# Optimization experiments

Measured on AMD Instinct MI355X. Metric: run time of the kernel, lower is better.

## Reference

```python
import jax, jax.numpy as jnp
import numpy as np
from jax import lax

K, N = 256, 65536

def setup_inputs() -> dict:
    key = jax.random.key(0)
    k1, k2, k3 = jax.random.split(key, 3)
    # obs: non-negative event counts [K, N]
    obs = jax.random.uniform(k1, (K, N), dtype=jnp.float32) * 4.0
    # Beta ~ U(1, 3) [K]
    Beta = 1.0 + 2.0 * jax.random.uniform(k2, (K,), dtype=jnp.float32)
    # Alpha ~ U(0, 0.01) [K, K]
    Alpha = 0.01 * jax.random.uniform(k3, (K, K), dtype=jnp.float32)
    return {"obs": obs, "Beta": Beta, "Alpha": Alpha}

def reference(obs, Beta, Alpha):
    # obs: [K, N], Beta: [K], Alpha: [K, K]
    Kk, Nn = obs.shape
    Mu0 = obs.mean(axis=1) / 10.0 + 0.01            # [K] background rate
    decay = jnp.exp(-Beta)                          # [K]

    # Exponential kernel sum S[t] = sum_{tp<t} obs[:,tp] * Beta * exp(-(t-tp)*Beta)
    # admits recursion H[t] = exp(-Beta) * (H[t-1] + obs[:, t-1]), S[t] = Beta * H[t]
    def step(h, o_prev):
        h_new = decay * (h + o_prev)
        return h_new, h_new

    _, H = lax.scan(step, jnp.zeros((Kk,), obs.dtype), obs[:, :Nn - 1].T)  # [N-1, K]
    S = H * Beta                                    # [N-1, K]
    # lam1[:, t] = softplus(Alpha @ S[t]) for t >= 1; lam1[:, 0] = 0 (by original code)
    lam = jax.nn.softplus(jnp.einsum('jk,tk->tj', Alpha, S))  # [N-1, K]
    lams1 = jnp.concatenate([jnp.zeros((Kk, 1), obs.dtype), lam.T], axis=1)  # [K, N]
    lams0 = jnp.broadcast_to(Mu0[:, None], (Kk, Nn))          # [K, N]

    Nloglams = obs * jnp.log(lams0 + lams1 + 1e-5)
    loglik = (Nloglams - lams0 - lams1).sum()
    return loglik, lams0, lams1
```

## Files before the change

### kernel.cpp

```cpp
#include <hip/hip_runtime.h>
#include <math.h>

#define KK 256
#define NN 65536
#define TT 64
#define WW 48
#define TPAD 264

typedef __bf16 bf16x8 __attribute__((ext_vector_type(8)));
typedef float f32x4 __attribute__((ext_vector_type(4)));

__global__ __launch_bounds__(256) void rowsum_kernel(const float* __restrict__ obs,
                                                     float* __restrict__ partial) {
  const int b = blockIdx.x;
  const int r = b >> 3, e = b & 7;
  const int tid = threadIdx.x;
  const float4* p = (const float4*)(obs + (size_t)r * NN + e * 8192) + tid;
  float s = 0.f;
#pragma unroll
  for (int i = 0; i < 8; ++i) {
    float4 v = p[i * 256];
    s += (v.x + v.y) + (v.z + v.w);
  }
  __shared__ float red[256];
  red[tid] = s;
  __syncthreads();
  for (int off = 128; off > 0; off >>= 1) {
    if (tid < off) red[tid] += red[tid + off];
    __syncthreads();
  }
  if (tid == 0) partial[b] = red[0];
}

__global__ __launch_bounds__(256) void prep_kernel(const float* __restrict__ Alpha,
                                                   const float* __restrict__ partial,
                                                   float* __restrict__ mu0,
                                                   __bf16* __restrict__ AlphaB,
                                                   float* __restrict__ out) {
  const int j = blockIdx.x;
  const int tid = threadIdx.x;
  AlphaB[(size_t)j * KK + tid] = (__bf16)Alpha[(size_t)j * KK + tid];
  if (tid == 0) {
    float s = 0.f;
#pragma unroll
    for (int i = 0; i < 8; ++i) s += partial[j * 8 + i];
    mu0[j] = s * (1.0f / NN) * 0.1f + 0.01f;
    if (j == 0) out[0] = 0.f;
  }
}

__global__ __launch_bounds__(256, 2) void main_kernel(const float* __restrict__ obs,
                                                      const float* __restrict__ Beta,
                                                      const float* __restrict__ mu0,
                                                      const __bf16* __restrict__ AlphaB,
                                                      float* __restrict__ out) {
  __shared__ __bf16 Slds[TT][TPAD];
  const int tid = threadIdx.x;
  const int t0 = blockIdx.x * TT;

  {
    const int k = tid;
    const float beta = Beta[k];
    const float decay = expf(-beta);
    const float* row = obs + (size_t)k * NN;
    float g = 0.f;
    if (t0 > 0) {
      const float4* p = (const float4*)(row + t0 - WW);
#pragma unroll
      for (int i = 0; i < WW / 4; ++i) {
        float4 v = p[i];
        g = decay * (g + v.x);
        g = decay * (g + v.y);
        g = decay * (g + v.z);
        g = decay * (g + v.w);
      }
    }
    Slds[0][k] = (__bf16)(beta * g);
    const float4* q = (const float4*)(row + t0);
#pragma unroll
    for (int i = 0; i < 15; ++i) {
      float4 v = q[i];
      g = decay * (g + v.x); Slds[4 * i + 1][k] = (__bf16)(beta * g);
      g = decay * (g + v.y); Slds[4 * i + 2][k] = (__bf16)(beta * g);
      g = decay * (g + v.z); Slds[4 * i + 3][k] = (__bf16)(beta * g);
      g = decay * (g + v.w); Slds[4 * i + 4][k] = (__bf16)(beta * g);
    }
    {
      float4 v = q[15];
      g = decay * (g + v.x); Slds[61][k] = (__bf16)(beta * g);
      g = decay * (g + v.y); Slds[62][k] = (__bf16)(beta * g);
      g = decay * (g + v.z); Slds[63][k] = (__bf16)(beta * g);
    }
  }
  __syncthreads();

  const int wave = tid >> 6;
  const int lane = tid & 63;
  const int lquad = lane >> 4;
  const int l16 = lane & 15;

  f32x4 acc[4][4];
#pragma unroll
  for (int a = 0; a < 4; ++a)
#pragma unroll
    for (int b = 0; b < 4; ++b) acc[a][b] = (f32x4){0.f, 0.f, 0.f, 0.f};

  const __bf16* Abase = AlphaB + (size_t)(wave * 64 + l16) * KK + lquad * 8;
  for (int k0 = 0; k0 < KK; k0 += 32) {
    bf16x8 afrag[4], bfrag[4];
#pragma unroll
    for (int js = 0; js < 4; ++js)
      afrag[js] = *(const bf16x8*)(Abase + (size_t)js * 16 * KK + k0);
#pragma unroll
    for (int ts = 0; ts < 4; ++ts)
      bfrag[ts] = *(const bf16x8*)&Slds[ts * 16 + l16][k0 + lquad * 8];
#pragma unroll
    for (int js = 0; js < 4; ++js)
#pragma unroll
      for (int ts = 0; ts < 4; ++ts)
        acc[js][ts] = __builtin_amdgcn_mfma_f32_16x16x32_bf16(
            afrag[js], bfrag[ts], acc[js][ts], 0, 0, 0);
  }

  float partial = 0.f;
  float* lams0 = out + 1;
  float* lams1 = out + 1 + (size_t)KK * NN;
#pragma unroll
  for (int js = 0; js < 4; ++js) {
#pragma unroll
    for (int r = 0; r < 4; ++r) {
      const int j = wave * 64 + js * 16 + lquad * 4 + r;
      const float m = mu0[j];
      const size_t rowoff = (size_t)j * NN + t0 + l16;
#pragma unroll
      for (int ts = 0; ts < 4; ++ts) {
        float v = acc[js][ts][r];
        float lam = v + __logf(1.f + __expf(-v));
        if (t0 + ts * 16 + l16 == 0) lam = 0.f;
        lams1[rowoff + ts * 16] = lam;
        lams0[rowoff + ts * 16] = m;
        const float o = obs[rowoff + ts * 16];
        partial += o * __logf(m + lam + 1e-5f) - m - lam;
      }
    }
  }

#pragma unroll
  for (int off = 32; off > 0; off >>= 1)
    partial += __shfl_down(partial, off, 64);
  if (lane == 0) atomicAdd(out, partial);
}

extern "C" void kernel_launch(void* const* d_in, const int* in_sizes, int n_in,
                              void* d_out, int out_size, void* d_ws, size_t ws_size,
                              hipStream_t stream) {
  const float* obs   = (const float*)d_in[0];
  const float* Beta  = (const float*)d_in[1];
  const float* Alpha = (const float*)d_in[2];
  float* out = (float*)d_out;

  float* partial = (float*)d_ws;
  float* mu0 = partial + 2048;
  __bf16* AlphaB = (__bf16*)(mu0 + 256);

  hipLaunchKernelGGL(rowsum_kernel, dim3(KK * 8), dim3(256), 0, stream, obs, partial);
  hipLaunchKernelGGL(prep_kernel, dim3(KK), dim3(256), 0, stream, Alpha, partial,
                     mu0, AlphaB, out);
  hipLaunchKernelGGL(main_kernel, dim3(NN / TT), dim3(256), 0, stream,
                     obs, Beta, mu0, AlphaB, out);
}
```

Measured before the change: 278.2 us.

## Transpose MFMA operands for vectorized epilogue stores and replace atomics with block partials

Swaps the MFMA operand order so each lane's accumulator holds four consecutive time steps, enabling 16-byte stores of lams0/lams1 and vector loads of obs. Replaces per-wave global atomicAdd with per-block partial sums written to workspace and a small finish kernel that reduces them, removing the zero-init from prep. Output pointers are offset by one float, so wide stores may be misaligned, and an extra kernel launch is added.

Result: slower. 288.7 us (+3.8%).

```diff
diff --git a/kernel.cpp b/kernel.cpp
--- a/kernel.cpp
+++ b/kernel.cpp
@@ -35,8 +35,7 @@
 __global__ __launch_bounds__(256) void prep_kernel(const float* __restrict__ Alpha,
                                                    const float* __restrict__ partial,
                                                    float* __restrict__ mu0,
-                                                   __bf16* __restrict__ AlphaB,
-                                                   float* __restrict__ out) {
+                                                   __bf16* __restrict__ AlphaB) {
   const int j = blockIdx.x;
   const int tid = threadIdx.x;
   AlphaB[(size_t)j * KK + tid] = (__bf16)Alpha[(size_t)j * KK + tid];
@@ -45,7 +44,6 @@
 #pragma unroll
     for (int i = 0; i < 8; ++i) s += partial[j * 8 + i];
     mu0[j] = s * (1.0f / NN) * 0.1f + 0.01f;
-    if (j == 0) out[0] = 0.f;
   }
 }
 
@@ -53,7 +51,8 @@
                                                       const float* __restrict__ Beta,
                                                       const float* __restrict__ mu0,
                                                       const __bf16* __restrict__ AlphaB,
-                                                      float* __restrict__ out) {
+                                                      float* __restrict__ out,
+                                                      float* __restrict__ bpart) {
   __shared__ __bf16 Slds[TT][TPAD];
   const int tid = threadIdx.x;
   const int t0 = blockIdx.x * TT;
@@ -107,48 +106,76 @@
 
   const __bf16* Abase = AlphaB + (size_t)(wave * 64 + l16) * KK + lquad * 8;
   for (int k0 = 0; k0 < KK; k0 += 32) {
-    bf16x8 afrag[4], bfrag[4];
+    bf16x8 afrag[4], sfrag[4];
 #pragma unroll
     for (int js = 0; js < 4; ++js)
       afrag[js] = *(const bf16x8*)(Abase + (size_t)js * 16 * KK + k0);
 #pragma unroll
     for (int ts = 0; ts < 4; ++ts)
-      bfrag[ts] = *(const bf16x8*)&Slds[ts * 16 + l16][k0 + lquad * 8];
-#pragma unroll
-    for (int js = 0; js < 4; ++js)
-#pragma unroll
-      for (int ts = 0; ts < 4; ++ts)
-        acc[js][ts] = __builtin_amdgcn_mfma_f32_16x16x32_bf16(
-            afrag[js], bfrag[ts], acc[js][ts], 0, 0, 0);
+      sfrag[ts] = *(const bf16x8*)&Slds[ts * 16 + l16][k0 + lquad * 8];
+#pragma unroll
+    for (int ts = 0; ts < 4; ++ts)
+#pragma unroll
+      for (int js = 0; js < 4; ++js)
+        acc[ts][js] = __builtin_amdgcn_mfma_f32_16x16x32_bf16(
+            sfrag[ts], afrag[js], acc[ts][js], 0, 0, 0);
   }
 
   float partial = 0.f;
   float* lams0 = out + 1;
   float* lams1 = out + 1 + (size_t)KK * NN;
-#pragma unroll
-  for (int js = 0; js < 4; ++js) {
-#pragma unroll
-    for (int r = 0; r < 4; ++r) {
-      const int j = wave * 64 + js * 16 + lquad * 4 + r;
-      const float m = mu0[j];
-      const size_t rowoff = (size_t)j * NN + t0 + l16;
-#pragma unroll
-      for (int ts = 0; ts < 4; ++ts) {
-        float v = acc[js][ts][r];
-        float lam = v + __logf(1.f + __expf(-v));
-        if (t0 + ts * 16 + l16 == 0) lam = 0.f;
-        lams1[rowoff + ts * 16] = lam;
-        lams0[rowoff + ts * 16] = m;
-        const float o = obs[rowoff + ts * 16];
-        partial += o * __logf(m + lam + 1e-5f) - m - lam;
+  float mj[4];
+#pragma unroll
+  for (int js = 0; js < 4; ++js) mj[js] = mu0[wave * 64 + js * 16 + l16];
+
+#pragma unroll
+  for (int ts = 0; ts < 4; ++ts) {
+    const int tb = t0 + ts * 16 + lquad * 4;
+#pragma unroll
+    for (int js = 0; js < 4; ++js) {
+      const int j = wave * 64 + js * 16 + l16;
+      const size_t off = (size_t)j * NN + tb;
+      f32x4 v = acc[ts][js];
+      f32x4 lam;
+#pragma unroll
+      for (int r = 0; r < 4; ++r) {
+        const float x = v[r];
+        lam[r] = x + __logf(1.f + __expf(-x));
       }
+      if (tb == 0) lam[0] = 0.f;
+      const float m = mj[js];
+      f32x4 mv = {m, m, m, m};
+      __builtin_memcpy(lams1 + off, &lam, sizeof(lam));
+      __builtin_memcpy(lams0 + off, &mv, sizeof(mv));
+      const f32x4 o = *(const f32x4*)(obs + off);
+#pragma unroll
+      for (int r = 0; r < 4; ++r)
+        partial += o[r] * __logf(m + lam[r] + 1e-5f) - m - lam[r];
     }
   }
 
 #pragma unroll
   for (int off = 32; off > 0; off >>= 1)
     partial += __shfl_down(partial, off, 64);
-  if (lane == 0) atomicAdd(out, partial);
+  __syncthreads();
+  float* red = (float*)&Slds[0][0];
+  if (lane == 0) red[wave] = partial;
+  __syncthreads();
+  if (tid == 0) bpart[blockIdx.x] = (red[0] + red[1]) + (red[2] + red[3]);
+}
+
+__global__ __launch_bounds__(256) void finish_kernel(const float* __restrict__ bpart,
+                                                     float* __restrict__ out) {
+  const int tid = threadIdx.x;
+  f32x4 v = ((const f32x4*)bpart)[tid];
+  float s = (v[0] + v[1]) + (v[2] + v[3]);
+#pragma unroll
+  for (int off = 32; off > 0; off >>= 1)
+    s += __shfl_down(s, off, 64);
+  __shared__ float red[4];
+  if ((tid & 63) == 0) red[tid >> 6] = s;
+  __syncthreads();
+  if (tid == 0) out[0] = (red[0] + red[1]) + (red[2] + red[3]);
 }
 
 extern "C" void kernel_launch(void* const* d_in, const int* in_sizes, int n_in,
@@ -162,10 +189,12 @@
   float* partial = (float*)d_ws;
   float* mu0 = partial + 2048;
   __bf16* AlphaB = (__bf16*)(mu0 + 256);
+  float* bpart = (float*)(AlphaB + (size_t)KK * KK);
 
   hipLaunchKernelGGL(rowsum_kernel, dim3(KK * 8), dim3(256), 0, stream, obs, partial);
   hipLaunchKernelGGL(prep_kernel, dim3(KK), dim3(256), 0, stream, Alpha, partial,
-                     mu0, AlphaB, out);
+                     mu0, AlphaB);
   hipLaunchKernelGGL(main_kernel, dim3(NN / TT), dim3(256), 0, stream,
-                     obs, Beta, mu0, AlphaB, out);
-}
+                     obs, Beta, mu0, AlphaB, out, bpart);
+  hipLaunchKernelGGL(finish_kernel, dim3(1), dim3(256), 0, stream, bpart, out);
+}
```
